# Performance work log

Measured on AMD Instinct MI355X. Metric: run time of the kernel, lower is better.

Reference implementation:

```python
import jax, jax.numpy as jnp
import numpy as np

EPS = 1e-5
C, FR, T = 256, 7, 251  # channel, frequency, time
B = 32


def _bn(x, p, axis):
    # p: stacked [gamma, beta, running_mean, running_var] (eval-mode BatchNorm)
    g, b, m, v = p
    scale = g * jax.lax.rsqrt(v + EPS)
    shape = [1] * x.ndim
    shape[axis] = -1
    return x * scale.reshape(shape) + (b - m * scale).reshape(shape)


def _branch(xr, qw, qbn, kw, kbn, lbn):
    # xr: [N, Cin, L]. conv1x1 (no bias) + BN1d over channel axis.
    q = _bn(jnp.einsum('oc,ncl->nol', qw, xr), qbn, 1)
    k = _bn(jnp.einsum('oc,ncl->nol', kw, xr), kbn, 1)
    # adaptive_avg_pool2d((1, L)) on [N,1,Cin,L]: mean over channel axis, identity on L
    qv = q.mean(axis=1)  # [N, L]
    kv = k.mean(axis=1)  # [N, L]
    logits = qv[:, :, None] * kv[:, None, :]  # outer product == matmul(q^T, k): [N, L, L]
    g, b, m, v = lbn[:, 0]  # BatchNorm2d(1), eval mode -> scalar affine
    scale = g * jax.lax.rsqrt(v + EPS)
    w = jax.nn.softmax(logits * scale + (b - m * scale), axis=-1)
    # einsum 'bhxy,ihh->bhxy' == v * sum_i diag(w_i); return the diagonal sum [L]
    return jnp.einsum('nii->i', w)


def setup_inputs() -> dict:
    key = jax.random.key(0)
    ks = jax.random.split(key, 20)

    def w(k, o, i):
        return jax.random.normal(k, (o, i), jnp.float32) * 0.05

    def bn(k, n):
        k1, k2, k3, k4 = jax.random.split(k, 4)
        gamma = 1.0 + 0.1 * jax.random.normal(k1, (n,), jnp.float32)
        beta = 0.1 * jax.random.normal(k2, (n,), jnp.float32)
        mean = 0.1 * jax.random.normal(k3, (n,), jnp.float32)
        var = jnp.abs(1.0 + 0.1 * jax.random.normal(k4, (n,), jnp.float32))
        return jnp.stack([gamma, beta, mean, var])

    return {
        'x': jax.random.normal(ks[0], (B, C, FR, T), jnp.float32),
        'qc_w': w(ks[1], T, T), 'qc_bn': bn(ks[2], T),
        'kc_w': w(ks[3], T, T), 'kc_bn': bn(ks[4], T),
        'lc_bn': bn(ks[5], 1),
        'qf_w': w(ks[6], C, C), 'qf_bn': bn(ks[7], C),
        'kf_w': w(ks[8], C, C), 'kf_bn': bn(ks[9], C),
        'lf_bn': bn(ks[10], 1),
        'qt_w': w(ks[11], C, C), 'qt_bn': bn(ks[12], C),
        'kt_w': w(ks[13], C, C), 'kt_bn': bn(ks[14], C),
        'lt_bn': bn(ks[15], 1),
        'v_w': w(ks[16], C, C),
        'v_b': 0.05 * jax.random.normal(ks[17], (C,), jnp.float32),
        'v_bn': bn(ks[18], C),
    }


def reference(x, qc_w, qc_bn, kc_w, kc_bn, lc_bn,
              qf_w, qf_bn, kf_w, kf_bn, lf_bn,
              qt_w, qt_bn, kt_w, kt_bn, lt_bn,
              v_w, v_b, v_bn):
    b = x.shape[0]
    # x: [B, C, FR, T]
    x_c = x.transpose(0, 2, 3, 1).reshape(b * FR, T, C)   # conv over T channels
    x_f = x.transpose(0, 2, 1, 3).reshape(b * FR, C, T)   # conv over C channels
    x_t = x.transpose(0, 3, 1, 2).reshape(b * T, C, FR)   # conv over C channels
    dc = _branch(x_c, qc_w, qc_bn, kc_w, kc_bn, lc_bn)    # [C] (attention over channel axis of v)
    df = _branch(x_f, qf_w, qf_bn, kf_w, kf_bn, lf_bn)    # [T]
    dt = _branch(x_t, qt_w, qt_bn, kt_w, kt_bn, lt_bn)    # [FR]
    v = _bn(jnp.einsum('oc,bcxy->boxy', v_w, x) + v_b[None, :, None, None], v_bn, 1)
    # v_c + v_f + v_t + x, where each v_* = v scaled by summed attention diagonal
    return v * (dc[None, :, None, None] + dt[None, None, :, None] + df[None, None, None, :]) + x
```

## Files before the change

### kernel.cpp

```cpp
#include <hip/hip_runtime.h>

typedef unsigned short u16;
typedef __attribute__((ext_vector_type(8))) short short8;
typedef __attribute__((ext_vector_type(4))) float float4v;
typedef __attribute__((ext_vector_type(4))) int int4v;
typedef __attribute__((ext_vector_type(2))) int int2v;

#define EPS 1e-5f
#define NC 256
#define NT 251
#define NF 7
#define NSP 1757
#define NB 32

#define OFF_QEC 0
#define OFF_KEC 256
#define OFF_QEF 512
#define OFF_KEF 768
#define OFF_QET 1024
#define OFF_KET 1280
#define OFF_VSC 1536
#define OFF_VOF 1792
#define OFF_CONST 2048
#define OFF_DC 2064
#define OFF_DF 2320
#define OFF_DT 2576
#define WS_END 2592
#define OFF_QT 2592
#define OFF_KT (OFF_QT+56320)
#define WS2_END (OFF_KT+56320)
#define OFF_WB16 WS2_END
#define WS3_END (WS2_END+32768)
#define OFF_QF2 WS3_END
#define OFF_KF2 (OFF_QF2+56320)
#define OFF_QCS (OFF_KF2+56320)
#define OFF_KCS (OFF_QCS+57344)
#define WS4_END (OFF_KCS+57344)
#define OFF_XB16 WS4_END
#define XB16_U32 (448*16384)
#define WS5_END (OFF_XB16 + XB16_U32)

#define XSW(kg, w) ((kg)*256 + ((w) ^ ((((kg)>>1)&3)<<3)))

__device__ __forceinline__ u16 f2b(float f) {
    unsigned int u = __float_as_uint(f);
    return (u16)((u + 0x7FFFu + ((u >> 16) & 1u)) >> 16);
}
__device__ __forceinline__ unsigned int pk2(float a, float b) {
    return (unsigned int)f2b(a) | ((unsigned int)f2b(b) << 16);
}

__global__ __launch_bounds__(256) void prep_kernel(
    const float* qc_w, const float* qc_bn, const float* kc_w, const float* kc_bn, const float* lc_bn,
    const float* qf_w, const float* qf_bn, const float* kf_w, const float* kf_bn, const float* lf_bn,
    const float* qt_w, const float* qt_bn, const float* kt_w, const float* kt_bn, const float* lt_bn,
    const float* v_b, const float* v_bn, const float* v_w, float* ws)
{
    int tid = threadIdx.x;
    int blk = blockIdx.x;
    __shared__ float sc[256];
    __shared__ float red[256];
    if (blk < 24) {
        int m = blk >> 2, j = blk & 3;
        const float* w; const float* bn; float* out; int O;
        switch (m) {
            case 0: w=qc_w; bn=qc_bn; out=ws+OFF_QEC; O=NT; break;
            case 1: w=kc_w; bn=kc_bn; out=ws+OFF_KEC; O=NT; break;
            case 2: w=qf_w; bn=qf_bn; out=ws+OFF_QEF; O=NC; break;
            case 3: w=kf_w; bn=kf_bn; out=ws+OFF_KEF; O=NC; break;
            case 4: w=qt_w; bn=qt_bn; out=ws+OFF_QET; O=NC; break;
            default: w=kt_w; bn=kt_bn; out=ws+OFF_KET; O=NC; break;
        }
        if (tid < O) sc[tid] = bn[tid] * rsqrtf(bn[3*O+tid] + EPS);
        __syncthreads();
        int tl = tid & 63, kc4 = tid >> 6;
        int t = j*64 + tl;
        float acc = 0.f;
        if (t < O) {
            #pragma unroll 8
            for (int o = kc4; o < O; o += 4)
                acc = fmaf(sc[o], w[(size_t)o*O + t], acc);
        }
        red[tid] = acc;
        __syncthreads();
        if (tid < 64) {
            int tt = j*64 + tid;
            if (tt < O)
                out[tt] = (red[tid] + red[tid+64] + red[tid+128] + red[tid+192]) / (float)O;
        }
        if (j == 0) {
            float bs = 0.f;
            if (tid < O) bs = bn[O+tid] - bn[2*O+tid]*sc[tid];
            __syncthreads();
            red[tid] = bs; __syncthreads();
            for (int s2 = 128; s2 > 0; s2 >>= 1) { if (tid < s2) red[tid] += red[tid+s2]; __syncthreads(); }
            if (tid == 0) ws[OFF_CONST+m] = red[0] / (float)O;
        }
    } else if (blk == 24) {
        if (tid < NC) {
            float s = v_bn[tid] * rsqrtf(v_bn[3*NC+tid] + EPS);
            ws[OFF_VSC+tid] = s;
            ws[OFF_VOF+tid] = v_bn[NC+tid] - v_bn[2*NC+tid]*s + v_b[tid]*s;
        }
        if (tid == 0) {
            ws[OFF_CONST+6] = lc_bn[0] * rsqrtf(lc_bn[3] + EPS);
            ws[OFF_CONST+7] = lf_bn[0] * rsqrtf(lf_bn[3] + EPS);
            ws[OFF_CONST+8] = lt_bn[0] * rsqrtf(lt_bn[3] + EPS);
        }
        for (int i = tid; i < WS_END - OFF_DC; i += 256) ws[OFF_DC + i] = 0.f;
    } else {
        u16* wb = (u16*)(ws + OFF_WB16);
        int base = (blk - 25) * 8192;
        for (int i4 = tid; i4 < 2048; i4 += 256) {
            int e = base + i4*4;
            int o = e >> 8, k = e & 255;
            float4v v = *(const float4v*)(v_w + e);
            u16 h0 = f2b(v.x), h1 = f2b(v.y), h2 = f2b(v.z), h3 = f2b(v.w);
            int r = ((o>>7)<<3) | (k>>5);
            int q = (((o>>4)&7)<<9) | (((k>>3)&3)<<7) | ((o&15)<<3) | (k&7);
            unsigned long long pk = (unsigned long long)h0 | ((unsigned long long)h1<<16)
                                  | ((unsigned long long)h2<<32) | ((unsigned long long)h3<<48);
            *(unsigned long long*)&wb[(r<<12) | q] = pk;
        }
    }
}

__global__ __launch_bounds__(512) void qv_kernel(const float* __restrict__ x,
                                                 float* __restrict__ ws, int pack)
{
    __shared__ float lds[8608];
    int tid = threadIdx.x;
    int blk = blockIdx.x;
    const float* cst = ws + OFF_CONST;

    if (blk < 1792) {
        int n = blk >> 3, cb = blk & 7;
        int b = n / NF, f = n % NF;
        const float* xb = x + (size_t)b*NC*NSP + (size_t)f*NT + (size_t)(cb*32)*NSP;
        if (tid < NT) lds[8096+tid] = ws[OFF_QEC+tid];
        else if (tid >= 256 && tid < 256+NT) lds[8352+tid-256] = ws[OFF_KEC+tid-256];
        int lr = tid >> 8, lane = tid & 255;
        #pragma unroll 4
        for (int i = 0; i < 16; ++i) {
            int r = 2*i + lr;
            if (lane < NT) lds[r*253 + lane] = xb[(size_t)r*NSP + lane];
        }
        __syncthreads();
        int r = tid >> 4, q = tid & 15;
        float qa = 0.f, ka = 0.f;
        #pragma unroll
        for (int i = 0; i < 16; ++i) {
            int t = q + 16*i;
            if (t < NT) {
                float xv = lds[r*253 + t];
                qa = fmaf(lds[8096+t], xv, qa);
                ka = fmaf(lds[8352+t], xv, ka);
            }
        }
        qa += __shfl_xor(qa, 1);  ka += __shfl_xor(ka, 1);
        qa += __shfl_xor(qa, 2);  ka += __shfl_xor(ka, 2);
        qa += __shfl_xor(qa, 4);  ka += __shfl_xor(ka, 4);
        qa += __shfl_xor(qa, 8);  ka += __shfl_xor(ka, 8);
        if (q == 0) {
            int ch = cb*32 + r;
            ws[OFF_QCS + n*256 + ch] = qa;
            ws[OFF_KCS + n*256 + ch] = ka;
        }
    } else {
        int fb = blk - 1792;
        int b = fb / 14, nchunk = fb % 14;
        int n0 = nchunk * 128;
        int spg = tid & 31, chg = tid >> 5;
        if (tid < 256) { lds[5120+tid] = ws[OFF_QEF+tid]; lds[5632+tid] = ws[OFF_QET+tid]; }
        else { int u = tid-256; lds[5376+u] = ws[OFF_KEF+u]; lds[5888+u] = ws[OFF_KET+u]; }
        __syncthreads();
        const size_t xbase = (size_t)b*NC*NSP;
        int sp0 = n0 + spg*4;
        bool full = (sp0 + 3 < NSP);
        unsigned int* ximg = nullptr;
        if (pack) ximg = (unsigned int*)(ws + OFF_XB16) + (size_t)(b*14 + nchunk)*16384;

        float qf[4]={0,0,0,0}, kf[4]={0,0,0,0}, qt[4]={0,0,0,0}, kt[4]={0,0,0,0};
        #pragma unroll
        for (int ii = 0; ii < 4; ++ii) {
            int ch0 = chg*16 + ii*4;
            float xv4[4][4];
            #pragma unroll
            for (int cc = 0; cc < 4; ++cc) {
                int ch = ch0 + cc;
                const float* xr = x + xbase + (size_t)ch*NSP + sp0;
                if (full) {
                    xv4[cc][0]=xr[0]; xv4[cc][1]=xr[1]; xv4[cc][2]=xr[2]; xv4[cc][3]=xr[3];
                } else {
                    #pragma unroll
                    for (int j = 0; j < 4; ++j) xv4[cc][j] = (sp0+j < NSP) ? xr[j] : 0.f;
                }
                float eqf = lds[5120+ch], ekf = lds[5376+ch];
                float eqt = lds[5632+ch], ekt = lds[5888+ch];
                #pragma unroll
                for (int j = 0; j < 4; ++j) {
                    qf[j] = fmaf(eqf, xv4[cc][j], qf[j]);
                    kf[j] = fmaf(ekf, xv4[cc][j], kf[j]);
                    qt[j] = fmaf(eqt, xv4[cc][j], qt[j]);
                    kt[j] = fmaf(ekt, xv4[cc][j], kt[j]);
                }
            }
            if (pack) {
                int kgsg = ch0 >> 2;
                int ks = kgsg >> 3, kgl = kgsg & 7;
                unsigned int* dst = ximg + ks*2048 + kgl*256 + spg*8;
                unsigned int pk[8];
                #pragma unroll
                for (int i = 0; i < 4; ++i) {
                    pk[i*2+0] = pk2(xv4[0][i], xv4[1][i]);
                    pk[i*2+1] = pk2(xv4[2][i], xv4[3][i]);
                }
                *(int4v*)&dst[0] = *(int4v*)&pk[0];
                *(int4v*)&dst[4] = *(int4v*)&pk[4];
            }
        }
        #pragma unroll
        for (int j = 0; j < 4; ++j) {
            qf[j] += __shfl_xor(qf[j], 32);
            kf[j] += __shfl_xor(kf[j], 32);
            qt[j] += __shfl_xor(qt[j], 32);
            kt[j] += __shfl_xor(kt[j], 32);
        }
        int wv = tid >> 6, ln = tid & 63;
        if (ln < 32) {
            int base = wv*640 + ln*20;
            #pragma unroll
            for (int j = 0; j < 4; ++j) {
                lds[base+j]    = qf[j];
                lds[base+4+j]  = kf[j];
                lds[base+8+j]  = qt[j];
                lds[base+12+j] = kt[j];
            }
        }
        __syncthreads();
        if (tid < 32) {
            float acc[16];
            #pragma unroll
            for (int j = 0; j < 16; ++j) acc[j] = 0.f;
            #pragma unroll
            for (int w = 0; w < 8; ++w) {
                int base = w*640 + tid*20;
                #pragma unroll
                for (int j = 0; j < 16; ++j) acc[j] += lds[base+j];
            }
            int sp0w = n0 + tid*4;
            #pragma unroll
            for (int j = 0; j < 4; ++j) {
                if (sp0w + j < NSP) {
                    size_t o = (size_t)b*1760 + sp0w + j;
                    ws[OFF_QF2 + o] = acc[j]    + cst[2];
                    ws[OFF_KF2 + o] = acc[4+j]  + cst[3];
                    ws[OFF_QT  + o] = acc[8+j]  + cst[4];
                    ws[OFF_KT  + o] = acc[12+j] + cst[5];
                }
            }
        }
    }
}

__global__ __launch_bounds__(256) void sm_kernel(float* __restrict__ ws)
{
    __shared__ float kv[NC];
    __shared__ float kv2[NT];
    __shared__ float dt_acc[NF];
    int tid = threadIdx.x, blk = blockIdx.x;
    const float* cst = ws + OFF_CONST;

    if (blk < 224) {
        int b = blk / NF, f = blk % NF;
        float qcv = ws[OFF_QCS + blk*256 + tid] + cst[0];
        float kcv = ws[OFF_KCS + blk*256 + tid] + cst[1];
        kv[tid] = kcv;
        float qfv = 0.f, kfv = 0.f;
        if (tid < NT) {
            size_t o = (size_t)b*1760 + f*NT + tid;
            qfv = ws[OFF_QF2 + o];
            kfv = ws[OFF_KF2 + o];
            kv2[tid] = kfv;
        }
        __syncthreads();
        {
            float s = cst[6];
            float qi = s * qcv;
            float m0=-1e30f, m1=-1e30f, m2=-1e30f, m3=-1e30f;
            #pragma unroll 2
            for (int jj = 0; jj < NC; jj += 4) {
                m0 = fmaxf(m0, qi*kv[jj]);
                m1 = fmaxf(m1, qi*kv[jj+1]);
                m2 = fmaxf(m2, qi*kv[jj+2]);
                m3 = fmaxf(m3, qi*kv[jj+3]);
            }
            float m = fmaxf(fmaxf(m0,m1), fmaxf(m2,m3));
            float d0=0.f, d1=0.f, d2=0.f, d3=0.f;
            #pragma unroll 2
            for (int jj = 0; jj < NC; jj += 4) {
                d0 += __expf(qi*kv[jj]   - m);
                d1 += __expf(qi*kv[jj+1] - m);
                d2 += __expf(qi*kv[jj+2] - m);
                d3 += __expf(qi*kv[jj+3] - m);
            }
            float den = (d0+d1)+(d2+d3);
            atomicAdd(&ws[OFF_DC + tid], __expf(qi*kcv - m)/den);
        }
        if (tid < NT) {
            float s = cst[7];
            float qi = s * qfv;
            float m0=-1e30f, m1=-1e30f, m2=-1e30f, m3=-1e30f;
            int jj = 0;
            #pragma unroll 2
            for (; jj + 3 < NT; jj += 4) {
                m0 = fmaxf(m0, qi*kv2[jj]);
                m1 = fmaxf(m1, qi*kv2[jj+1]);
                m2 = fmaxf(m2, qi*kv2[jj+2]);
                m3 = fmaxf(m3, qi*kv2[jj+3]);
            }
            for (; jj < NT; ++jj) m0 = fmaxf(m0, qi*kv2[jj]);
            float m = fmaxf(fmaxf(m0,m1), fmaxf(m2,m3));
            float d0=0.f, d1=0.f, d2=0.f, d3=0.f;
            jj = 0;
            #pragma unroll 2
            for (; jj + 3 < NT; jj += 4) {
                d0 += __expf(qi*kv2[jj]   - m);
                d1 += __expf(qi*kv2[jj+1] - m);
                d2 += __expf(qi*kv2[jj+2] - m);
                d3 += __expf(qi*kv2[jj+3] - m);
            }
            for (; jj < NT; ++jj) d0 += __expf(qi*kv2[jj] - m);
            float den = (d0+d1)+(d2+d3);
            atomicAdd(&ws[OFF_DF + tid], __expf(qi*kfv - m)/den);
        }
    } else {
        int b = blk - 224;
        if (tid < NF) dt_acc[tid] = 0.f;
        __syncthreads();
        if (tid < NT) {
            float s = cst[8];
            float q[NF], k[NF];
            #pragma unroll
            for (int i = 0; i < NF; ++i) {
                size_t o = (size_t)b*1760 + i*NT + tid;
                q[i] = ws[OFF_QT + o];
                k[i] = ws[OFF_KT + o];
            }
            #pragma unroll
            for (int i = 0; i < NF; ++i) {
                float qi = s * q[i];
                float m = -1e30f;
                #pragma unroll
                for (int j = 0; j < NF; ++j) m = fmaxf(m, qi*k[j]);
                float den = 0.f;
                #pragma unroll
                for (int j = 0; j < NF; ++j) den += __expf(qi*k[j] - m);
                atomicAdd(&dt_acc[i], __expf(qi*k[i] - m)/den);
            }
        }
        __syncthreads();
        if (tid < NF) atomicAdd(&ws[OFF_DT + tid], dt_acc[tid]);
    }
}

__global__ __launch_bounds__(512) void qkt_kernel(const float* __restrict__ x,
                                                  float* __restrict__ ws, int fuse_t)
{
    __shared__ float kv[NC];
    __shared__ float p0[512], p1[512], p2[512], p3[512];
    int tid = threadIdx.x;
    int bid = blockIdx.x;
    int n = bid >> 1, role = bid & 1;
    int b = n / NF, f = n % NF;
    const float* xb = x + (size_t)b*NC*NSP + (size_t)f*NT;
    const float* cst = ws + OFF_CONST;
    int half = tid >> 8, lid = tid & 255;

    if (role == 0) {
        const float* xrow = xb + (size_t)lid*NSP;
        const float* qeC = ws + OFF_QEC;  const float* keC = ws + OFF_KEC;
        float qc = 0.f, kc = 0.f;
        int t0 = half ? 126 : 0, t1 = half ? NT : 126;
        #pragma unroll 16
        for (int t = t0; t < t1; ++t) {
            float xv = xrow[t];
            qc = fmaf(qeC[t], xv, qc);
            kc = fmaf(keC[t], xv, kc);
        }
        p0[tid] = qc; p1[tid] = kc;
        __syncthreads();
        if (tid < 256) {
            qc = p0[tid] + p0[tid+256] + cst[0];
            kc = p1[tid] + p1[tid+256] + cst[1];
            kv[tid] = kc;
        }
        __syncthreads();
        if (tid < 256) {
            float s = cst[6];
            float qi = s * qc;
            float m0=-1e30f, m1=-1e30f, m2=-1e30f, m3=-1e30f;
            #pragma unroll 2
            for (int jj = 0; jj < NC; jj += 4) {
                m0 = fmaxf(m0, qi*kv[jj]);
                m1 = fmaxf(m1, qi*kv[jj+1]);
                m2 = fmaxf(m2, qi*kv[jj+2]);
                m3 = fmaxf(m3, qi*kv[jj+3]);
            }
            float m = fmaxf(fmaxf(m0,m1), fmaxf(m2,m3));
            float d0=0.f, d1=0.f, d2=0.f, d3=0.f;
            #pragma unroll 2
            for (int jj = 0; jj < NC; jj += 4) {
                d0 += __expf(qi*kv[jj]   - m);
                d1 += __expf(qi*kv[jj+1] - m);
                d2 += __expf(qi*kv[jj+2] - m);
                d3 += __expf(qi*kv[jj+3] - m);
            }
            float den = (d0+d1)+(d2+d3);
            atomicAdd(&ws[OFF_DC + tid], __expf(qi*kv[tid] - m)/den);
        }
    } else {
        float qf=0.f, kf=0.f, qt=0.f, kt=0.f;
        if (lid < NT) {
            const float* xc = xb + lid + (size_t)(half*128)*NSP;
            const float* qeF = ws + OFF_QEF + half*128;  const float* keF = ws + OFF_KEF + half*128;
            const float* qeT = ws + OFF_QET + half*128;  const float* keT = ws + OFF_KET + half*128;
            #pragma unroll 8
            for (int ch = 0; ch < 128; ++ch) {
                float xv = xc[(size_t)ch*NSP];
                qf = fmaf(qeF[ch], xv, qf);
                kf = fmaf(keF[ch], xv, kf);
                qt = fmaf(qeT[ch], xv, qt);
                kt = fmaf(keT[ch], xv, kt);
            }
        }
        p0[tid]=qf; p1[tid]=kf; p2[tid]=qt; p3[tid]=kt;
        __syncthreads();
        float qfv=0.f, kfv=0.f;
        if (tid < NT) {
            qfv = p0[tid] + p0[tid+256] + cst[2];
            kfv = p1[tid] + p1[tid+256] + cst[3];
            float qtv = p2[tid] + p2[tid+256] + cst[4];
            float ktv = p3[tid] + p3[tid+256] + cst[5];
            kv[tid] = kfv;
            if (fuse_t) {
                ws[OFF_QT + ((size_t)b*NT + tid)*NF + f] = qtv;
                ws[OFF_KT + ((size_t)b*NT + tid)*NF + f] = ktv;
            }
        }
        __syncthreads();
        if (tid < NT) {
            float s = cst[7];
            float qi = s * qfv;
            float m0=-1e30f, m1=-1e30f, m2=-1e30f, m3=-1e30f;
            int jj = 0;
            #pragma unroll 2
            for (; jj + 3 < NT; jj += 4) {
                m0 = fmaxf(m0, qi*kv[jj]);
                m1 = fmaxf(m1, qi*kv[jj+1]);
                m2 = fmaxf(m2, qi*kv[jj+2]);
                m3 = fmaxf(m3, qi*kv[jj+3]);
            }
            for (; jj < NT; ++jj) m0 = fmaxf(m0, qi*kv[jj]);
            float m = fmaxf(fmaxf(m0,m1), fmaxf(m2,m3));
            float d0=0.f, d1=0.f, d2=0.f, d3=0.f;
            jj = 0;
            #pragma unroll 2
            for (; jj + 3 < NT; jj += 4) {
                d0 += __expf(qi*kv[jj]   - m);
                d1 += __expf(qi*kv[jj+1] - m);
                d2 += __expf(qi*kv[jj+2] - m);
                d3 += __expf(qi*kv[jj+3] - m);
            }
            for (; jj < NT; ++jj) d0 += __expf(qi*kv[jj] - m);
            float den = (d0+d1)+(d2+d3);
            atomicAdd(&ws[OFF_DF + tid], __expf(qi*kfv - m)/den);
        }
    }
}

__global__ __launch_bounds__(256) void tsm_kernel(float* __restrict__ ws)
{
    __shared__ float dt_acc[NF];
    int tid = threadIdx.x, b = blockIdx.x;
    if (tid < NF) dt_acc[tid] = 0.f;
    __syncthreads();
    if (tid < NT) {
        float s = ws[OFF_CONST+8];
        const float* qp = ws + OFF_QT + ((size_t)b*NT + tid)*NF;
        const float* kp = ws + OFF_KT + ((size_t)b*NT + tid)*NF;
        float q[NF], k[NF];
        #pragma unroll
        for (int i = 0; i < NF; ++i) { q[i] = qp[i]; k[i] = kp[i]; }
        #pragma unroll
        for (int i = 0; i < NF; ++i) {
            float qi = s * q[i];
            float m = -1e30f;
            #pragma unroll
            for (int j = 0; j < NF; ++j) m = fmaxf(m, qi*k[j]);
            float den = 0.f;
            #pragma unroll
            for (int j = 0; j < NF; ++j) den += __expf(qi*k[j] - m);
            atomicAdd(&dt_acc[i], __expf(qi*k[i] - m)/den);
        }
    }
    __syncthreads();
    if (tid < NF) atomicAdd(&ws[OFF_DT + tid], dt_acc[tid]);
}

__global__ __launch_bounds__(256) void t_kernel(const float* __restrict__ x, float* __restrict__ ws)
{
    __shared__ float qs[32*NF], ks[32*NF], dt_acc[NF];
    int tid = threadIdx.x;
    int b  = blockIdx.x >> 3;
    int t0 = (blockIdx.x & 7) * 32;
    int tl = tid & 31, fr = tid >> 5;
    int t = t0 + tl;
    bool act = (fr < NF) && (t < NT);
    if (tid < NF) dt_acc[tid] = 0.f;

    float aq = 0.f, ak = 0.f;
    const float* qeT = ws + OFF_QET;
    const float* keT = ws + OFF_KET;
    if (act) {
        const float* xr = x + (size_t)b*NC*NSP + fr*NT + t;
        #pragma unroll 8
        for (int ch = 0; ch < NC; ++ch) {
            float xv = xr[(size_t)ch*NSP];
            aq = fmaf(qeT[ch], xv, aq);
            ak = fmaf(keT[ch], xv, ak);
        }
    }
    __syncthreads();
    if (act) {
        qs[tl*NF + fr] = aq + ws[OFF_CONST+4];
        ks[tl*NF + fr] = ak + ws[OFF_CONST+5];
    }
    __syncthreads();
    if (act) {
        float s = ws[OFF_CONST+8];
        float qi = s * qs[tl*NF + fr];
        float m = -1e30f;
        #pragma unroll
        for (int j = 0; j < NF; ++j) m = fmaxf(m, qi*ks[tl*NF + j]);
        float den = 0.f;
        #pragma unroll
        for (int j = 0; j < NF; ++j) den += __expf(qi*ks[tl*NF + j] - m);
        atomicAdd(&dt_acc[fr], __expf(qi*ks[tl*NF + fr] - m)/den);
    }
    __syncthreads();
    if (tid < NF) atomicAdd(&ws[OFF_DT + tid], dt_acc[tid]);
}

__global__ __launch_bounds__(256, 3) void main2_kernel(
    const float* __restrict__ x, const float* __restrict__ ws, float* __restrict__ out)
{
    __shared__ float vsL[128], voL[128], dcL[128], dtfL[128];
    int tid = threadIdx.x;
    int flat = blockIdx.x;
    int xcd = flat & 7, idx = flat >> 3;
    int pair = xcd*56 + (idx >> 1);
    int o0 = (idx & 1) * 128;
    int n0 = (pair % 14) * 128;
    int b  = pair / 14;
    const size_t xbase = (size_t)b * NC * NSP;

    if (tid < 128) {
        int o = o0 + tid;
        vsL[tid] = ws[OFF_VSC+o];
        voL[tid] = ws[OFF_VOF+o];
        dcL[tid] = ws[OFF_DC+o];
        int nn = n0 + tid; if (nn > NSP-1) nn = NSP-1;
        int ff = nn / NT, tt = nn - ff*NT;
        dtfL[tid] = ws[OFF_DT+ff] + ws[OFF_DF+tt];
    }
    __syncthreads();

    int wv = tid >> 6, ln = tid & 63;
    int quad = ln >> 4, l16 = ln & 15;
    int wr = wv >> 1, wc = wv & 1;

    const u16* wimg = (const u16*)(ws + OFF_WB16) + (size_t)(o0 >> 7) * 32768;
    const unsigned int* ximg = (const unsigned int*)(ws + OFF_XB16)
                             + (size_t)(b*14 + (n0 >> 7)) * 16384;

    float4v acc[4][4] = {};

    #pragma unroll 2
    for (int ks = 0; ks < 8; ++ks) {
        short8 afr[4], bfr[4];
        #pragma unroll
        for (int fr = 0; fr < 4; ++fr)
            afr[fr] = *(const short8*)&wimg[ks*4096 + (wr*4+fr)*512 + ln*8];
        #pragma unroll
        for (int fc = 0; fc < 4; ++fc) {
            int nn = wc*64 + fc*16 + l16;
            int2v lo = *(const int2v*)&ximg[ks*2048 + (2*quad)*256 + 2*nn];
            int2v hi = *(const int2v*)&ximg[ks*2048 + (2*quad+1)*256 + 2*nn];
            union { int i4[4]; short8 v; } u;
            u.i4[0] = lo.x; u.i4[1] = lo.y; u.i4[2] = hi.x; u.i4[3] = hi.y;
            bfr[fc] = u.v;
        }
        #pragma unroll
        for (int fr = 0; fr < 4; ++fr)
            #pragma unroll
            for (int fc = 0; fc < 4; ++fc)
                acc[fr][fc] = __builtin_amdgcn_mfma_f32_16x16x32_bf16(
                    afr[fr], bfr[fc], acc[fr][fc], 0, 0, 0);
    }

    #pragma unroll
    for (int fr = 0; fr < 4; ++fr) {
        #pragma unroll
        for (int r = 0; r < 4; ++r) {
            int ol = wr*64 + fr*16 + quad*4 + r;
            int o = o0 + ol;
            float vs = vsL[ol], vo = voL[ol], dcv = dcL[ol];
            const size_t orow = xbase + (size_t)o*NSP;
            #pragma unroll
            for (int fc = 0; fc < 4; ++fc) {
                int nl = wc*64 + fc*16 + l16;
                int nn = n0 + nl;
                if (nn < NSP) {
                    size_t gi = orow + nn;
                    out[gi] = (acc[fr][fc][r]*vs + vo)*(dcv + dtfL[nl]) + x[gi];
                }
            }
        }
    }
}

template<int WBF>
__global__ __launch_bounds__(256) void main_kernel(
    const float* __restrict__ x, const float* __restrict__ vw,
    const float* __restrict__ ws, float* __restrict__ out)
{
    __shared__ u16 Ws[2][4096];
    __shared__ unsigned int Xs[2][2048];
    __shared__ float vsL[128], voL[128], dcL[128], dtfL[128];

    int tid = threadIdx.x;
    int flat = blockIdx.x;
    int xcd = flat & 7, idx = flat >> 3;
    int pair = xcd*56 + (idx >> 1);
    int o0 = (idx & 1) * 128;
    int n0 = (pair % 14) * 128;
    int b  = pair / 14;
    const size_t xbase = (size_t)b * NC * NSP;

    if (tid < 128) {
        int o = o0 + tid;
        vsL[tid] = ws[OFF_VSC+o];
        voL[tid] = ws[OFF_VOF+o];
        dcL[tid] = ws[OFF_DC+o];
        int nn = n0 + tid; if (nn > NSP-1) nn = NSP-1;
        int ff = nn / NT, tt = nn - ff*NT;
        dtfL[tid] = ws[OFF_DT+ff] + ws[OFF_DF+tt];
    }

    int wv = tid >> 6, ln = tid & 63;
    int quad = ln >> 4, l16 = ln & 15;
    int wr = wv >> 1, wc = wv & 1;

    float4v acc[4][4] = {};

    int kgs = tid >> 5, nbs = tid & 31;
    int oo = tid >> 1, half = tid & 1;

    const u16* wbg = nullptr;
    if constexpr (WBF) wbg = (const u16*)(ws + OFF_WB16) + (size_t)(o0 >> 7) * 32768;

    int4v wA, wB;
    float wf[16];
    float xv[4][4];

    auto loadW = [&](int ks) {
        if constexpr (WBF) {
            const int4v* wsrc = (const int4v*)(wbg + (size_t)ks*4096);
            wA = wsrc[tid]; wB = wsrc[256 + tid];
        } else {
            const float* wr4 = vw + (size_t)(o0+oo)*NC + ks*32 + half*16;
            #pragma unroll
            for (int c = 0; c < 16; ++c) wf[c] = wr4[c];
        }
    };
    auto loadX = [&](int ks) {
        int nbase = n0 + nbs*4;
        const float* xr = x + xbase + (size_t)(ks*32 + kgs*4)*NSP + nbase;
        if (nbase + 3 < NSP) {
            #pragma unroll
            for (int rr = 0; rr < 4; ++rr)
                #pragma unroll
                for (int i = 0; i < 4; ++i)
                    xv[rr][i] = xr[(size_t)rr*NSP + i];
        } else {
            #pragma unroll
            for (int rr = 0; rr < 4; ++rr)
                #pragma unroll
                for (int i = 0; i < 4; ++i)
                    xv[rr][i] = (nbase + i < NSP) ? xr[(size_t)rr*NSP + i] : 0.f;
        }
    };
    auto storeWX = [&](int bufi) {
        if constexpr (WBF) {
            *(int4v*)&Ws[bufi][tid*8]        = wA;
            *(int4v*)&Ws[bufi][2048 + tid*8] = wB;
        } else {
            union { u16 us[16]; short8 v[2]; } wb;
            #pragma unroll
            for (int c = 0; c < 16; ++c) wb.us[c] = f2b(wf[c]);
            int frg = oo >> 4, o16 = oo & 15;
            #pragma unroll
            for (int qq = 0; qq < 2; ++qq) {
                int qd = 2*half + qq;
                *(short8*)&Ws[bufi][frg*512 + qd*128 + o16*8] = wb.v[qq];
            }
        }
        unsigned int pk[8];
        #pragma unroll
        for (int i = 0; i < 4; ++i)
            #pragma unroll
            for (int jp = 0; jp < 2; ++jp)
                pk[i*2+jp] = pk2(xv[2*jp][i], xv[2*jp+1][i]);
        *(int4v*)&Xs[bufi][XSW(kgs, nbs*8)]     = *(int4v*)&pk[0];
        *(int4v*)&Xs[bufi][XSW(kgs, nbs*8 + 4)] = *(int4v*)&pk[4];
    };

    loadW(0); loadX(0);
    storeWX(0);
    __syncthreads();

    for (int ks = 0; ks < 8; ++ks) {
        int cur = ks & 1;
        if (ks < 7) { loadW(ks+1); loadX(ks+1); }

        short8 afr[4], bfr[4];
        #pragma unroll
        for (int fr = 0; fr < 4; ++fr)
            afr[fr] = *(short8*)&Ws[cur][(wr*4+fr)*512 + ln*8];
        #pragma unroll
        for (int fc = 0; fc < 4; ++fc) {
            int nn = wc*64 + fc*16 + l16;
            int2v lo = *(int2v*)&Xs[cur][XSW(2*quad,   2*nn)];
            int2v hi = *(int2v*)&Xs[cur][XSW(2*quad+1, 2*nn)];
            union { int i4[4]; short8 v; } u;
            u.i4[0] = lo.x; u.i4[1] = lo.y; u.i4[2] = hi.x; u.i4[3] = hi.y;
            bfr[fc] = u.v;
        }
        #pragma unroll
        for (int fr = 0; fr < 4; ++fr)
            #pragma unroll
            for (int fc = 0; fc < 4; ++fc)
                acc[fr][fc] = __builtin_amdgcn_mfma_f32_16x16x32_bf16(
                    afr[fr], bfr[fc], acc[fr][fc], 0, 0, 0);

        if (ks < 7) storeWX(cur ^ 1);
        __syncthreads();
    }

    #pragma unroll
    for (int fr = 0; fr < 4; ++fr) {
        #pragma unroll
        for (int r = 0; r < 4; ++r) {
            int ol = wr*64 + fr*16 + quad*4 + r;
            int o = o0 + ol;
            float vs = vsL[ol], vo = voL[ol], dcv = dcL[ol];
            const size_t orow = xbase + (size_t)o*NSP;
            #pragma unroll
            for (int fc = 0; fc < 4; ++fc) {
                int nl = wc*64 + fc*16 + l16;
                int nn = n0 + nl;
                if (nn < NSP) {
                    size_t gi = orow + nn;
                    out[gi] = (acc[fr][fc][r]*vs + vo)*(dcv + dtfL[nl]) + x[gi];
                }
            }
        }
    }
}

extern "C" void kernel_launch(void* const* d_in, const int* in_sizes, int n_in,
                              void* d_out, int out_size, void* d_ws, size_t ws_size,
                              hipStream_t stream)
{
    const float* x    = (const float*)d_in[0];
    const float* qc_w = (const float*)d_in[1];  const float* qc_bn = (const float*)d_in[2];
    const float* kc_w = (const float*)d_in[3];  const float* kc_bn = (const float*)d_in[4];
    const float* lc_bn= (const float*)d_in[5];
    const float* qf_w = (const float*)d_in[6];  const float* qf_bn = (const float*)d_in[7];
    const float* kf_w = (const float*)d_in[8];  const float* kf_bn = (const float*)d_in[9];
    const float* lf_bn= (const float*)d_in[10];
    const float* qt_w = (const float*)d_in[11]; const float* qt_bn = (const float*)d_in[12];
    const float* kt_w = (const float*)d_in[13]; const float* kt_bn = (const float*)d_in[14];
    const float* lt_bn= (const float*)d_in[15];
    const float* v_w  = (const float*)d_in[16]; const float* v_b   = (const float*)d_in[17];
    const float* v_bn = (const float*)d_in[18];
    float* ws = (float*)d_ws;
    float* out = (float*)d_out;

    int fuse_t = (ws_size >= (size_t)WS2_END * sizeof(float)) ? 1 : 0;
    int wbf    = (ws_size >= (size_t)WS3_END * sizeof(float)) ? 1 : 0;
    int newq   = (ws_size >= (size_t)WS4_END * sizeof(float)) ? 1 : 0;
    int xb     = (ws_size >= (size_t)WS5_END * sizeof(float)) ? 1 : 0;

    prep_kernel<<<wbf ? 33 : 25, 256, 0, stream>>>(qc_w,qc_bn,kc_w,kc_bn,lc_bn,
                                                   qf_w,qf_bn,kf_w,kf_bn,lf_bn,
                                                   qt_w,qt_bn,kt_w,kt_bn,lt_bn,
                                                   v_b,v_bn,v_w,ws);
    if (newq) {
        qv_kernel<<<2240, 512, 0, stream>>>(x, ws, xb);
        sm_kernel<<<256, 256, 0, stream>>>(ws);
    } else {
        qkt_kernel<<<NB*NF*2, 512, 0, stream>>>(x, ws, fuse_t);
        if (fuse_t) tsm_kernel<<<NB, 256, 0, stream>>>(ws);
        else        t_kernel<<<NB*8, 256, 0, stream>>>(x, ws);
    }
    if (xb && wbf)
        main2_kernel<<<896, 256, 0, stream>>>(x, ws, out);
    else if (wbf)
        main_kernel<1><<<896, 256, 0, stream>>>(x, v_w, ws, out);
    else
        main_kernel<0><<<896, 256, 0, stream>>>(x, v_w, ws, out);
}
```

Baseline: 224.7 us.

## Software-pipeline main GEMM loads and fix LDS bank conflicts in reductions

The main GEMM loop now double-buffers its global fragment loads, fetching step ks+1 while the MFMAs for step ks run. The per-block scale and offset loads are kept in registers and written to LDS only after the MMA loop, so the barrier no longer sits before the compute. In qv_kernel the channel-branch reduction becomes a segmented per-thread sum over a padded 257 stride with an LDS cross-segment reduction, and the f/t partial sums use a transposed LDS layout to cut bank conflicts. These changes raise register pressure, which may hurt occupancy under launch_bounds(256,3), and add a barrier and LDS traffic in qv_kernel.

```diff
diff --git a/kernel.cpp b/kernel.cpp
--- a/kernel.cpp
+++ b/kernel.cpp
@@ -128,7 +128,7 @@
 __global__ __launch_bounds__(512) void qv_kernel(const float* __restrict__ x,
                                                  float* __restrict__ ws, int pack)
 {
-    __shared__ float lds[8608];
+    __shared__ float lds[9760];
     int tid = threadIdx.x;
     int blk = blockIdx.x;
     const float* cst = ws + OFF_CONST;
@@ -137,34 +137,36 @@
         int n = blk >> 3, cb = blk & 7;
         int b = n / NF, f = n % NF;
         const float* xb = x + (size_t)b*NC*NSP + (size_t)f*NT + (size_t)(cb*32)*NSP;
-        if (tid < NT) lds[8096+tid] = ws[OFF_QEC+tid];
-        else if (tid >= 256 && tid < 256+NT) lds[8352+tid-256] = ws[OFF_KEC+tid-256];
+        if (tid < NT) lds[8224+tid] = ws[OFF_QEC+tid];
+        else if (tid >= 256 && tid < 256+NT) lds[8480+tid-256] = ws[OFF_KEC+tid-256];
         int lr = tid >> 8, lane = tid & 255;
         #pragma unroll 4
         for (int i = 0; i < 16; ++i) {
             int r = 2*i + lr;
-            if (lane < NT) lds[r*253 + lane] = xb[(size_t)r*NSP + lane];
-        }
-        __syncthreads();
-        int r = tid >> 4, q = tid & 15;
+            if (lane < NT) lds[r*257 + lane] = xb[(size_t)r*NSP + lane];
+        }
+        __syncthreads();
+        int r = tid & 31, seg = tid >> 5;
+        int t0 = seg*16, t1 = (seg == 15) ? NT : t0+16;
         float qa = 0.f, ka = 0.f;
-        #pragma unroll
-        for (int i = 0; i < 16; ++i) {
-            int t = q + 16*i;
-            if (t < NT) {
-                float xv = lds[r*253 + t];
-                qa = fmaf(lds[8096+t], xv, qa);
-                ka = fmaf(lds[8352+t], xv, ka);
-            }
-        }
-        qa += __shfl_xor(qa, 1);  ka += __shfl_xor(ka, 1);
-        qa += __shfl_xor(qa, 2);  ka += __shfl_xor(ka, 2);
-        qa += __shfl_xor(qa, 4);  ka += __shfl_xor(ka, 4);
-        qa += __shfl_xor(qa, 8);  ka += __shfl_xor(ka, 8);
-        if (q == 0) {
-            int ch = cb*32 + r;
-            ws[OFF_QCS + n*256 + ch] = qa;
-            ws[OFF_KCS + n*256 + ch] = ka;
+        #pragma unroll 4
+        for (int t = t0; t < t1; ++t) {
+            float xv = lds[r*257 + t];
+            qa = fmaf(lds[8224+t], xv, qa);
+            ka = fmaf(lds[8480+t], xv, ka);
+        }
+        lds[8736 + seg*32 + r] = qa;
+        lds[9248 + seg*32 + r] = ka;
+        __syncthreads();
+        if (tid < 64) {
+            int rr = tid & 31, which = tid >> 5;
+            int base = 8736 + which*512 + rr;
+            float s = 0.f;
+            #pragma unroll
+            for (int sg = 0; sg < 16; ++sg) s += lds[base + sg*32];
+            int ch = cb*32 + rr;
+            if (which == 0) ws[OFF_QCS + n*256 + ch] = s;
+            else            ws[OFF_KCS + n*256 + ch] = s;
         }
     } else {
         int fb = blk - 1792;
@@ -228,25 +230,23 @@
         }
         int wv = tid >> 6, ln = tid & 63;
         if (ln < 32) {
-            int base = wv*640 + ln*20;
             #pragma unroll
             for (int j = 0; j < 4; ++j) {
-                lds[base+j]    = qf[j];
-                lds[base+4+j]  = kf[j];
-                lds[base+8+j]  = qt[j];
-                lds[base+12+j] = kt[j];
+                lds[(j)*256     + wv*32 + ln] = qf[j];
+                lds[(4+j)*256   + wv*32 + ln] = kf[j];
+                lds[(8+j)*256   + wv*32 + ln] = qt[j];
+                lds[(12+j)*256  + wv*32 + ln] = kt[j];
             }
         }
         __syncthreads();
         if (tid < 32) {
             float acc[16];
             #pragma unroll
-            for (int j = 0; j < 16; ++j) acc[j] = 0.f;
-            #pragma unroll
-            for (int w = 0; w < 8; ++w) {
-                int base = w*640 + tid*20;
+            for (int v = 0; v < 16; ++v) {
+                float s = 0.f;
                 #pragma unroll
-                for (int j = 0; j < 16; ++j) acc[j] += lds[base+j];
+                for (int w = 0; w < 8; ++w) s += lds[v*256 + w*32 + tid];
+                acc[v] = s;
             }
             int sp0w = n0 + tid*4;
             #pragma unroll
@@ -565,16 +565,16 @@
     int b  = pair / 14;
     const size_t xbase = (size_t)b * NC * NSP;
 
+    float evs=0.f, evo=0.f, edc=0.f, edtf=0.f;
     if (tid < 128) {
         int o = o0 + tid;
-        vsL[tid] = ws[OFF_VSC+o];
-        voL[tid] = ws[OFF_VOF+o];
-        dcL[tid] = ws[OFF_DC+o];
+        evs = ws[OFF_VSC+o];
+        evo = ws[OFF_VOF+o];
+        edc = ws[OFF_DC+o];
         int nn = n0 + tid; if (nn > NSP-1) nn = NSP-1;
         int ff = nn / NT, tt = nn - ff*NT;
-        dtfL[tid] = ws[OFF_DT+ff] + ws[OFF_DF+tt];
-    }
-    __syncthreads();
+        edtf = ws[OFF_DT+ff] + ws[OFF_DF+tt];
+    }
 
     int wv = tid >> 6, ln = tid & 63;
     int quad = ln >> 4, l16 = ln & 15;
@@ -585,29 +585,41 @@
                              + (size_t)(b*14 + (n0 >> 7)) * 16384;
 
     float4v acc[4][4] = {};
-
-    #pragma unroll 2
-    for (int ks = 0; ks < 8; ++ks) {
-        short8 afr[4], bfr[4];
+    short8 afr[2][4];
+    int2v blo[2][4], bhi[2][4];
+
+    auto LF = [&](int ks, int s) {
         #pragma unroll
         for (int fr = 0; fr < 4; ++fr)
-            afr[fr] = *(const short8*)&wimg[ks*4096 + (wr*4+fr)*512 + ln*8];
+            afr[s][fr] = *(const short8*)&wimg[ks*4096 + (wr*4+fr)*512 + ln*8];
         #pragma unroll
         for (int fc = 0; fc < 4; ++fc) {
             int nn = wc*64 + fc*16 + l16;
-            int2v lo = *(const int2v*)&ximg[ks*2048 + (2*quad)*256 + 2*nn];
-            int2v hi = *(const int2v*)&ximg[ks*2048 + (2*quad+1)*256 + 2*nn];
+            blo[s][fc] = *(const int2v*)&ximg[ks*2048 + (2*quad)*256 + 2*nn];
+            bhi[s][fc] = *(const int2v*)&ximg[ks*2048 + (2*quad+1)*256 + 2*nn];
+        }
+    };
+
+    LF(0, 0);
+    #pragma unroll
+    for (int ks = 0; ks < 8; ++ks) {
+        const int cur = ks & 1;
+        if (ks < 7) LF(ks+1, cur ^ 1);
+        #pragma unroll
+        for (int fc = 0; fc < 4; ++fc) {
             union { int i4[4]; short8 v; } u;
-            u.i4[0] = lo.x; u.i4[1] = lo.y; u.i4[2] = hi.x; u.i4[3] = hi.y;
-            bfr[fc] = u.v;
-        }
-        #pragma unroll
-        for (int fr = 0; fr < 4; ++fr)
-            #pragma unroll
-            for (int fc = 0; fc < 4; ++fc)
+            u.i4[0] = blo[cur][fc].x; u.i4[1] = blo[cur][fc].y;
+            u.i4[2] = bhi[cur][fc].x; u.i4[3] = bhi[cur][fc].y;
+            short8 bv = u.v;
+            #pragma unroll
+            for (int fr = 0; fr < 4; ++fr)
                 acc[fr][fc] = __builtin_amdgcn_mfma_f32_16x16x32_bf16(
-                    afr[fr], bfr[fc], acc[fr][fc], 0, 0, 0);
-    }
+                    afr[cur][fr], bv, acc[fr][fc], 0, 0, 0);
+        }
+    }
+
+    if (tid < 128) { vsL[tid]=evs; voL[tid]=evo; dcL[tid]=edc; dtfL[tid]=edtf; }
+    __syncthreads();
 
     #pragma unroll
     for (int fr = 0; fr < 4; ++fr) {
```

After: 225.8 us. No clear change (+0.5%).
